# Kernel tuning notes

Hardware: AMD Instinct MI355X
Metric: run time of the kernel (lower is better)

The kernel has to match this reference:

```python
import jax, jax.numpy as jnp
import numpy as np

B, N, C = 4, 2048, 768
H = 12
D = C // H  # head_dim = 64
SCALE = D ** -0.5


def setup_inputs() -> dict:
    key = jax.random.key(0)
    ks = jax.random.split(key, 9)
    x = jax.random.normal(ks[0], (B, N, C), dtype=jnp.float32)
    k_in = jax.random.normal(ks[1], (B, N, C), dtype=jnp.float32)
    v_in = jax.random.normal(ks[2], (B, N, C), dtype=jnp.float32)
    rel_pos_bias = jax.random.normal(ks[3], (H, N, N), dtype=jnp.float32)
    # learned params (nn.Linear stores weight [out, in]; y = x @ W.T + b)
    s = C ** -0.5
    Wq = jax.random.normal(ks[4], (C, C), dtype=jnp.float32) * s
    Wk = jax.random.normal(ks[5], (C, C), dtype=jnp.float32) * s
    Wv = jax.random.normal(ks[6], (C, C), dtype=jnp.float32) * s
    Wp = jax.random.normal(ks[7], (C, C), dtype=jnp.float32) * s
    bp = jax.random.normal(ks[8], (C,), dtype=jnp.float32) * 0.01
    return {"x": x, "k_in": k_in, "v_in": v_in, "rel_pos_bias": rel_pos_bias,
            "Wq": Wq, "Wk": Wk, "Wv": Wv, "Wp": Wp, "bp": bp}


def reference(x, k_in, v_in, rel_pos_bias, Wq, Wk, Wv, Wp, bp):
    # linear projections (no q/k/v bias since qkv_bias=False)
    q = jnp.einsum('bnc,dc->bnd', x, Wq)      # [B,N,C]
    k = jnp.einsum('bnc,dc->bnd', k_in, Wk)   # [B,Nk,C]
    v = jnp.einsum('bnc,dc->bnd', v_in, Wv)   # [B,Nv,C]
    # split heads -> [B,H,N,D]
    q = q.reshape(B, N, H, D).transpose(0, 2, 1, 3) * SCALE
    k = k.reshape(B, -1, H, D).transpose(0, 2, 1, 3)
    v = v.reshape(B, -1, H, D).transpose(0, 2, 1, 3)
    attn = jnp.einsum('bhnd,bhmd->bhnm', q, k)          # [B,H,N,Nk]
    attn = attn + rel_pos_bias[None]                    # additive rel-pos bias
    attn = jax.nn.softmax(attn, axis=-1)
    out = jnp.einsum('bhnm,bhmd->bhnd', attn, v)        # [B,H,N,D]
    out = out.transpose(0, 2, 1, 3).reshape(B, N, C)
    return jnp.einsum('bnc,dc->bnd', out, Wp) + bp
```

## Files before the change

### kernel.cpp

```cpp
#include <hip/hip_runtime.h>
#include <stdint.h>
#include <stddef.h>

#define B_ 4
#define N_ 2048
#define C_ 768
#define H_ 12
#define M_ (B_ * N_)

typedef __attribute__((ext_vector_type(8))) short bf16x8_t;
typedef __attribute__((ext_vector_type(4))) float f32x4_t;

__device__ __forceinline__ unsigned pack2_bf16(float f0, float f1) {
  unsigned u0 = __builtin_bit_cast(unsigned, f0) + 0x8000u;
  unsigned u1 = __builtin_bit_cast(unsigned, f1) + 0x8000u;
  return __builtin_amdgcn_perm(u1, u0, 0x07060302u);
}

__device__ __forceinline__ short f2bf(float f) {
  unsigned u = __builtin_bit_cast(unsigned, f);
  u = (u + 0x7FFFu + ((u >> 16) & 1u)) >> 16;
  return (short)u;
}
__device__ __forceinline__ short f2bf_fast(float f) {
  return (short)((__builtin_bit_cast(unsigned, f) + 0x8000u) >> 16);
}

__device__ __forceinline__ void gload_lds16(const short* g, const short* l) {
  __builtin_amdgcn_global_load_lds(
      (const __attribute__((address_space(1))) void*)g,
      (__attribute__((address_space(3))) void*)l, 16, 0, 0);
}

#define XV 1572864
#define WV 147456
__global__ __launch_bounds__(256) void cvt_all(
    const float* __restrict__ x, const float* __restrict__ kin, const float* __restrict__ vin,
    const float* __restrict__ wq, const float* __restrict__ wk, const float* __restrict__ wv,
    const float* __restrict__ wp,
    unsigned short* __restrict__ xb, unsigned short* __restrict__ kb, unsigned short* __restrict__ vb,
    unsigned short* __restrict__ wqb, unsigned short* __restrict__ wkb, unsigned short* __restrict__ wvb,
    unsigned short* __restrict__ wpb)
{
  int i = blockIdx.x * 256 + threadIdx.x;
  const float* s; unsigned short* d; int off;
  if      (i < XV)            { s = x;   d = xb;  off = i; }
  else if (i < 2 * XV)        { s = kin; d = kb;  off = i - XV; }
  else if (i < 3 * XV)        { s = vin; d = vb;  off = i - 2 * XV; }
  else if (i < 3 * XV + WV)   { s = wq;  d = wqb; off = i - 3 * XV; }
  else if (i < 3 * XV + 2*WV) { s = wk;  d = wkb; off = i - 3 * XV - WV; }
  else if (i < 3 * XV + 3*WV) { s = wv;  d = wvb; off = i - 3 * XV - 2 * WV; }
  else                        { s = wp;  d = wpb; off = i - 3 * XV - 3 * WV; }
  float4 v = ((const float4*)s)[off];
  uint2 p;
  p.x = pack2_bf16(v.x, v.y);
  p.y = pack2_bf16(v.z, v.w);
  ((uint2*)d)[off] = p;
}

__global__ __launch_bounds__(256) void proj_qkv(
    const short* __restrict__ xb, const short* __restrict__ kb, const short* __restrict__ vb,
    const short* __restrict__ wqb, const short* __restrict__ wkb, const short* __restrict__ wvb,
    short* __restrict__ q_ws, short* __restrict__ k_ws, short* __restrict__ vt_ws)
{
  const int z = blockIdx.z;
  const short* A = (z == 0) ? xb : (z == 1) ? kb : vb;
  const short* W = (z == 0) ? wqb : (z == 1) ? wkb : wvb;
  const int m0 = blockIdx.x * 128;
  const int n0 = blockIdx.y * 128;

  __shared__ __align__(16) short smem[128 * 136];
  short* As = smem;
  short* Bs = smem + 128 * 64;

  const int t = threadIdx.x;
  const int w = t >> 6, L = t & 63, L15 = L & 15, quad = L >> 4;
  const int wm = w & 1, wn = w >> 1;

  f32x4_t acc[4][4] = {};

  const short* ga = A + (size_t)(m0 + w * 32 + (L >> 3)) * C_ + (L & 7) * 8;
  const short* gb = W + (size_t)(n0 + w * 32 + (L >> 3)) * C_ + (L & 7) * 8;
  const short* la = As + (w * 32) * 64;
  const short* lb = Bs + (w * 32) * 64;

  for (int k0 = 0; k0 < C_; k0 += 64) {
    __syncthreads();
    #pragma unroll
    for (int i = 0; i < 4; ++i) {
      gload_lds16(ga + (size_t)i * 8 * C_ + k0, la + i * 512);
      gload_lds16(gb + (size_t)i * 8 * C_ + k0, lb + i * 512);
    }
    __syncthreads();
    #pragma unroll
    for (int kk = 0; kk < 2; ++kk) {
      bf16x8_t af[4], bf[4];
      #pragma unroll
      for (int mt = 0; mt < 4; ++mt)
        af[mt] = *(const bf16x8_t*)&As[(wm * 64 + mt * 16 + L15) * 64 + kk * 32 + quad * 8];
      #pragma unroll
      for (int nt = 0; nt < 4; ++nt)
        bf[nt] = *(const bf16x8_t*)&Bs[(wn * 64 + nt * 16 + L15) * 64 + kk * 32 + quad * 8];
      #pragma unroll
      for (int mt = 0; mt < 4; ++mt)
        #pragma unroll
        for (int nt = 0; nt < 4; ++nt)
          acc[mt][nt] = __builtin_amdgcn_mfma_f32_16x16x32_bf16(af[mt], bf[nt], acc[mt][nt], 0, 0, 0);
    }
  }

  if (z != 2) {
    short* outp = (z == 0) ? q_ws : k_ws;
    const float mul = (z == 0) ? 0.125f : 1.0f;
    #pragma unroll
    for (int mt = 0; mt < 4; ++mt) {
      const int m_base = m0 + wm * 64 + mt * 16 + quad * 4;
      #pragma unroll
      for (int nt = 0; nt < 4; ++nt) {
        const int c = n0 + wn * 64 + nt * 16 + L15;
        const int h = c >> 6, d = c & 63;
        #pragma unroll
        for (int r = 0; r < 4; ++r) {
          const int m = m_base + r;
          const int b = m >> 11, n = m & 2047;
          outp[((size_t)(b * H_ + h) * N_ + n) * 64 + d] = f2bf(acc[mt][nt][r] * mul);
        }
      }
    }
  } else {
    __syncthreads();
    #pragma unroll
    for (int mt = 0; mt < 4; ++mt) {
      const int ml = wm * 64 + mt * 16 + quad * 4;
      #pragma unroll
      for (int nt = 0; nt < 4; ++nt) {
        const int cl = wn * 64 + nt * 16 + L15;
        #pragma unroll
        for (int r = 0; r < 4; ++r)
          smem[cl * 136 + ml + r] = f2bf(acc[mt][nt][r]);
      }
    }
    __syncthreads();
    const int bb = m0 >> 11;
    const int nn0 = m0 & 2047;
    #pragma unroll
    for (int pp = 0; pp < 8; ++pp) {
      const int cl = pp * 16 + (t >> 4);
      const int mg = t & 15;
      const uint4 val = *(const uint4*)&smem[cl * 136 + mg * 8];
      const int cg = n0 + cl;
      *(uint4*)&vt_ws[(((size_t)(bb * H_ + (cg >> 6))) * 64 + (cg & 63)) * N_ + nn0 + mg * 8] = val;
    }
  }
}

__global__ __launch_bounds__(256, 3) void attn(
    const short* __restrict__ q_ws, const short* __restrict__ k_ws,
    const short* __restrict__ vt_ws, const float* __restrict__ rpb,
    short* __restrict__ attn_out)
{
  const int p  = blockIdx.x;
  const int lw = (p & 7) * 96 + (p >> 3);
  const int h  = lw >> 6;
  const int xl = lw & 63;
  const int b  = xl & 3;
  const int m0 = (xl >> 2) * 128;
  const int bh = b * H_ + h;

  __shared__ __align__(16) short Ks [64 * 64];
  __shared__ __align__(16) short Vts[64 * 64];
  __shared__ __align__(16) short Ps [4][32 * 64];

  const int t = threadIdx.x;
  const int w = t >> 6, L = t & 63, L15 = L & 15, quad = L >> 4;
  const int sr  = t >> 2;
  const int scb = (t & 3) << 5;
  const int swz_w = (sr & 7) << 4;

  const short* qp  = q_ws  + ((size_t)bh * N_ + m0) * 64;
  const short* kp  = k_ws  + (size_t)bh * N_ * 64;
  const short* vtp = vt_ws + (size_t)bh * 64 * N_;
  const float* bpb = rpb + (size_t)h * N_ * N_;

  bf16x8_t aq[2][2];
  #pragma unroll
  for (int mt = 0; mt < 2; ++mt)
    #pragma unroll
    for (int kk = 0; kk < 2; ++kk)
      aq[mt][kk] = *(const bf16x8_t*)(qp + (size_t)(w * 32 + mt * 16 + L15) * 64 + kk * 32 + quad * 8);

  f32x4_t o[2][4] = {};
  float psum[2][4] = {};

  for (int kv0 = 0; kv0 < N_; kv0 += 64) {
    __syncthreads();
    {
      const short* gk = kp + (size_t)(kv0 + sr) * 64 + (scb >> 1);
      const uint4 k0 = *(const uint4*)gk;
      const uint4 k1 = *(const uint4*)(gk + 8);
      const short* gv = vtp + (size_t)sr * N_ + kv0 + (scb >> 1);
      const uint4 v0 = *(const uint4*)gv;
      const uint4 v1 = *(const uint4*)(gv + 8);
      *(uint4*)((char*)Ks  + sr * 128 + (scb ^ swz_w))        = k0;
      *(uint4*)((char*)Ks  + sr * 128 + ((scb + 16) ^ swz_w)) = k1;
      *(uint4*)((char*)Vts + sr * 128 + (scb ^ swz_w))        = v0;
      *(uint4*)((char*)Vts + sr * 128 + ((scb + 16) ^ swz_w)) = v1;
    }
    float bias[2][4][4];
    {
      const float* bq = bpb + (size_t)(m0 + w * 32 + quad * 4) * N_ + kv0 + L15;
      #pragma unroll
      for (int mt = 0; mt < 2; ++mt)
        #pragma unroll
        for (int r = 0; r < 4; ++r)
          #pragma unroll
          for (int nt = 0; nt < 4; ++nt)
            bias[mt][nt][r] = bq[(size_t)(mt * 16 + r) * N_ + nt * 16];
    }
    __syncthreads();

    f32x4_t s[2][4];
    #pragma unroll
    for (int nt = 0; nt < 4; ++nt) {
      const int row = nt * 16 + L15;
      const char* kbp = (const char*)Ks + row * 128;
      const int sx = (row & 7) << 4;
      const bf16x8_t b0 = *(const bf16x8_t*)(kbp + ((quad * 16) ^ sx));
      const bf16x8_t b1 = *(const bf16x8_t*)(kbp + ((64 + quad * 16) ^ sx));
      #pragma unroll
      for (int mt = 0; mt < 2; ++mt) {
        f32x4_t sv = {bias[mt][nt][0], bias[mt][nt][1], bias[mt][nt][2], bias[mt][nt][3]};
        sv = __builtin_amdgcn_mfma_f32_16x16x32_bf16(aq[mt][0], b0, sv, 0, 0, 0);
        s[mt][nt] = __builtin_amdgcn_mfma_f32_16x16x32_bf16(aq[mt][1], b1, sv, 0, 0, 0);
      }
    }

    #pragma unroll
    for (int mt = 0; mt < 2; ++mt)
      #pragma unroll
      for (int nt = 0; nt < 4; ++nt)
        #pragma unroll
        for (int r = 0; r < 4; ++r) {
          const float e = __expf(s[mt][nt][r]);
          psum[mt][r] += e;
          const int qrow = mt * 16 + quad * 4 + r;
          const int cb = (nt * 32 + L15 * 2) ^ ((qrow & 7) << 4);
          *(short*)((char*)Ps[w] + qrow * 128 + cb) = f2bf_fast(e);
        }

    #pragma unroll
    for (int kk = 0; kk < 2; ++kk) {
      bf16x8_t pa[2];
      #pragma unroll
      for (int mt = 0; mt < 2; ++mt) {
        const int row = mt * 16 + L15;
        pa[mt] = *(const bf16x8_t*)((char*)Ps[w] + row * 128 +
                                    ((kk * 64 + quad * 16) ^ ((row & 7) << 4)));
      }
      #pragma unroll
      for (int nt = 0; nt < 4; ++nt) {
        const int row = nt * 16 + L15;
        const bf16x8_t vbf = *(const bf16x8_t*)((char*)Vts + row * 128 +
                                                ((kk * 64 + quad * 16) ^ ((row & 7) << 4)));
        #pragma unroll
        for (int mt = 0; mt < 2; ++mt)
          o[mt][nt] = __builtin_amdgcn_mfma_f32_16x16x32_bf16(pa[mt], vbf, o[mt][nt], 0, 0, 0);
      }
    }
  }

  #pragma unroll
  for (int mt = 0; mt < 2; ++mt)
    #pragma unroll
    for (int r = 0; r < 4; ++r) {
      float v = psum[mt][r];
      v += __shfl_xor(v, 1);
      v += __shfl_xor(v, 2);
      v += __shfl_xor(v, 4);
      v += __shfl_xor(v, 8);
      psum[mt][r] = 1.0f / v;
    }

  #pragma unroll
  for (int mt = 0; mt < 2; ++mt) {
    const int n_base = m0 + w * 32 + mt * 16 + quad * 4;
    #pragma unroll
    for (int nt = 0; nt < 4; ++nt)
      #pragma unroll
      for (int r = 0; r < 4; ++r) {
        const float v = o[mt][nt][r] * psum[mt][r];
        attn_out[((size_t)(b * N_ + n_base + r)) * C_ + h * 64 + nt * 16 + L15] = f2bf(v);
      }
  }
}

__global__ __launch_bounds__(256) void proj_out(
    const short* __restrict__ Abf, const short* __restrict__ wpb,
    const float* __restrict__ bpv, float* __restrict__ out)
{
  const int m0 = blockIdx.x * 128;
  const int n0 = blockIdx.y * 128;

  __shared__ short As[128 * 64];
  __shared__ short Bs[128 * 64];

  const int t = threadIdx.x;
  const int w = t >> 6, L = t & 63, L15 = L & 15, quad = L >> 4;
  const int wm = w & 1, wn = w >> 1;

  f32x4_t acc[4][4] = {};

  const short* ga = Abf + (size_t)(m0 + w * 32 + (L >> 3)) * C_ + (L & 7) * 8;
  const short* gb = wpb + (size_t)(n0 + w * 32 + (L >> 3)) * C_ + (L & 7) * 8;
  const short* la = &As[(w * 32) * 64];
  const short* lb = &Bs[(w * 32) * 64];

  for (int k0 = 0; k0 < C_; k0 += 64) {
    __syncthreads();
    #pragma unroll
    for (int i = 0; i < 4; ++i) {
      gload_lds16(ga + (size_t)i * 8 * C_ + k0, la + i * 512);
      gload_lds16(gb + (size_t)i * 8 * C_ + k0, lb + i * 512);
    }
    __syncthreads();
    #pragma unroll
    for (int kk = 0; kk < 2; ++kk) {
      bf16x8_t af[4], bf[4];
      #pragma unroll
      for (int mt = 0; mt < 4; ++mt)
        af[mt] = *(const bf16x8_t*)&As[(wm * 64 + mt * 16 + L15) * 64 + kk * 32 + quad * 8];
      #pragma unroll
      for (int nt = 0; nt < 4; ++nt)
        bf[nt] = *(const bf16x8_t*)&Bs[(wn * 64 + nt * 16 + L15) * 64 + kk * 32 + quad * 8];
      #pragma unroll
      for (int mt = 0; mt < 4; ++mt)
        #pragma unroll
        for (int nt = 0; nt < 4; ++nt)
          acc[mt][nt] = __builtin_amdgcn_mfma_f32_16x16x32_bf16(af[mt], bf[nt], acc[mt][nt], 0, 0, 0);
    }
  }

  #pragma unroll
  for (int mt = 0; mt < 4; ++mt) {
    const int m_base = m0 + wm * 64 + mt * 16 + quad * 4;
    #pragma unroll
    for (int nt = 0; nt < 4; ++nt) {
      const int c = n0 + wn * 64 + nt * 16 + L15;
      const float bb = bpv[c];
      #pragma unroll
      for (int r = 0; r < 4; ++r)
        out[(size_t)(m_base + r) * C_ + c] = acc[mt][nt][r] + bb;
    }
  }
}

extern "C" void kernel_launch(void* const* d_in, const int* in_sizes, int n_in,
                              void* d_out, int out_size, void* d_ws, size_t ws_size,
                              hipStream_t stream) {
  const float* x    = (const float*)d_in[0];
  const float* k_in = (const float*)d_in[1];
  const float* v_in = (const float*)d_in[2];
  const float* rpb  = (const float*)d_in[3];
  const float* Wq   = (const float*)d_in[4];
  const float* Wk   = (const float*)d_in[5];
  const float* Wv   = (const float*)d_in[6];
  const float* Wp   = (const float*)d_in[7];
  const float* bp   = (const float*)d_in[8];
  float* out = (float*)d_out;

  const size_t SZ = (size_t)B_ * H_ * N_ * 64 * sizeof(short);
  const size_t WSZ = (size_t)C_ * C_ * sizeof(short);
  char* ws = (char*)d_ws;
  short* q_ws  = (short*)(ws);
  short* k_ws  = (short*)(ws + SZ);
  short* vt_ws = (short*)(ws + 2 * SZ);
  short* ao_ws = (short*)(ws + 3 * SZ);
  short* xb    = (short*)(ws + 4 * SZ);
  short* kb    = (short*)(ws + 5 * SZ);
  short* vb    = (short*)(ws + 6 * SZ);
  short* wqb   = (short*)(ws + 7 * SZ);
  short* wkb   = (short*)(ws + 7 * SZ + WSZ);
  short* wvb   = (short*)(ws + 7 * SZ + 2 * WSZ);
  short* wpb   = (short*)(ws + 7 * SZ + 3 * WSZ);

  cvt_all<<<(3 * XV + 4 * WV + 255) / 256, 256, 0, stream>>>(
      x, k_in, v_in, Wq, Wk, Wv, Wp,
      (unsigned short*)xb, (unsigned short*)kb, (unsigned short*)vb,
      (unsigned short*)wqb, (unsigned short*)wkb, (unsigned short*)wvb, (unsigned short*)wpb);
  proj_qkv<<<dim3(M_ / 128, C_ / 128, 3), 256, 0, stream>>>(
      xb, kb, vb, wqb, wkb, wvb, q_ws, k_ws, vt_ws);
  attn<<<dim3(B_ * (N_ / 128) * H_), 256, 0, stream>>>(q_ws, k_ws, vt_ws, rpb, ao_ws);
  proj_out<<<dim3(M_ / 128, C_ / 128), 256, 0, stream>>>(ao_ws, wpb, bp, out);
}
```

Measured before the change: 473.0 us.

## Double-buffer K/V tiles with direct global-to-LDS loads and prefetch bias

The attention kernel now keeps two LDS buffers for the K and V^T tiles and fills them with direct global-to-LDS loads (gload_lds16). The next tile is issued while the current one is being computed, and the loop needs only one barrier per iteration. Bias values for the next tile are loaded into registers after the QK MFMAs, which hides the latency of the large relative-position-bias stream. MFMA sections are wrapped in s_setprio raises. The cost is doubled LDS for K/V and more live registers, and the change depends on gload_lds16 handling its wait counts correctly before the barrier.

```diff
diff --git a/kernel.cpp b/kernel.cpp
--- a/kernel.cpp
+++ b/kernel.cpp
@@ -167,21 +167,23 @@
   const int m0 = (xl >> 2) * 128;
   const int bh = b * H_ + h;
 
-  __shared__ __align__(16) short Ks [64 * 64];
-  __shared__ __align__(16) short Vts[64 * 64];
+  __shared__ __align__(16) short Ks [2][64 * 64];
+  __shared__ __align__(16) short Vts[2][64 * 64];
   __shared__ __align__(16) short Ps [4][32 * 64];
 
   const int t = threadIdx.x;
   const int w = t >> 6, L = t & 63, L15 = L & 15, quad = L >> 4;
-  const int sr  = t >> 2;
-  const int scb = (t & 3) << 5;
-  const int swz_w = (sr & 7) << 4;
 
   const short* qp  = q_ws  + ((size_t)bh * N_ + m0) * 64;
   const short* kp  = k_ws  + (size_t)bh * N_ * 64;
   const short* vtp = vt_ws + (size_t)bh * 64 * N_;
   const float* bpb = rpb + (size_t)h * N_ * N_;
 
+  const int srow8 = L >> 3;
+  const int scolS = ((L & 7) ^ srow8) * 8;
+  const short* gk_base = kp  + (size_t)(w * 16 + srow8) * 64 + scolS;
+  const short* gv_base = vtp + (size_t)(w * 16 + srow8) * N_ + scolS;
+
   bf16x8_t aq[2][2];
   #pragma unroll
   for (int mt = 0; mt < 2; ++mt)
@@ -189,41 +191,44 @@
     for (int kk = 0; kk < 2; ++kk)
       aq[mt][kk] = *(const bf16x8_t*)(qp + (size_t)(w * 32 + mt * 16 + L15) * 64 + kk * 32 + quad * 8);
 
+  const float* bq = bpb + (size_t)(m0 + w * 32 + quad * 4) * N_ + L15;
+
   f32x4_t o[2][4] = {};
   float psum[2][4] = {};
-
-  for (int kv0 = 0; kv0 < N_; kv0 += 64) {
-    __syncthreads();
-    {
-      const short* gk = kp + (size_t)(kv0 + sr) * 64 + (scb >> 1);
-      const uint4 k0 = *(const uint4*)gk;
-      const uint4 k1 = *(const uint4*)(gk + 8);
-      const short* gv = vtp + (size_t)sr * N_ + kv0 + (scb >> 1);
-      const uint4 v0 = *(const uint4*)gv;
-      const uint4 v1 = *(const uint4*)(gv + 8);
-      *(uint4*)((char*)Ks  + sr * 128 + (scb ^ swz_w))        = k0;
-      *(uint4*)((char*)Ks  + sr * 128 + ((scb + 16) ^ swz_w)) = k1;
-      *(uint4*)((char*)Vts + sr * 128 + (scb ^ swz_w))        = v0;
-      *(uint4*)((char*)Vts + sr * 128 + ((scb + 16) ^ swz_w)) = v1;
-    }
-    float bias[2][4][4];
-    {
-      const float* bq = bpb + (size_t)(m0 + w * 32 + quad * 4) * N_ + kv0 + L15;
-      #pragma unroll
-      for (int mt = 0; mt < 2; ++mt)
-        #pragma unroll
-        for (int r = 0; r < 4; ++r)
-          #pragma unroll
-          for (int nt = 0; nt < 4; ++nt)
-            bias[mt][nt][r] = bq[(size_t)(mt * 16 + r) * N_ + nt * 16];
-    }
-    __syncthreads();
+  float bias[2][4][4];
+
+  #pragma unroll
+  for (int i = 0; i < 2; ++i) {
+    gload_lds16(gk_base + (size_t)i * 8 * 64, &Ks[0][w * 1024 + i * 512]);
+    gload_lds16(gv_base + (size_t)i * 8 * N_, &Vts[0][w * 1024 + i * 512]);
+  }
+  #pragma unroll
+  for (int mt = 0; mt < 2; ++mt)
+    #pragma unroll
+    for (int r = 0; r < 4; ++r)
+      #pragma unroll
+      for (int nt = 0; nt < 4; ++nt)
+        bias[mt][nt][r] = bq[(size_t)(mt * 16 + r) * N_ + nt * 16];
+  __syncthreads();
+
+  for (int T = 0; T < 32; ++T) {
+    const int cur = T & 1, nxt = cur ^ 1;
+
+    if (T < 31) {
+      const int kv1 = (T + 1) * 64;
+      #pragma unroll
+      for (int i = 0; i < 2; ++i) {
+        gload_lds16(gk_base + (size_t)(kv1 + i * 8) * 64, &Ks[nxt][w * 1024 + i * 512]);
+        gload_lds16(gv_base + (size_t)i * 8 * N_ + kv1,   &Vts[nxt][w * 1024 + i * 512]);
+      }
+    }
 
     f32x4_t s[2][4];
+    __builtin_amdgcn_s_setprio(1);
     #pragma unroll
     for (int nt = 0; nt < 4; ++nt) {
       const int row = nt * 16 + L15;
-      const char* kbp = (const char*)Ks + row * 128;
+      const char* kbp = (const char*)Ks[cur] + row * 128;
       const int sx = (row & 7) << 4;
       const bf16x8_t b0 = *(const bf16x8_t*)(kbp + ((quad * 16) ^ sx));
       const bf16x8_t b1 = *(const bf16x8_t*)(kbp + ((64 + quad * 16) ^ sx));
@@ -233,6 +238,18 @@
         sv = __builtin_amdgcn_mfma_f32_16x16x32_bf16(aq[mt][0], b0, sv, 0, 0, 0);
         s[mt][nt] = __builtin_amdgcn_mfma_f32_16x16x32_bf16(aq[mt][1], b1, sv, 0, 0, 0);
       }
+    }
+    __builtin_amdgcn_s_setprio(0);
+
+    if (T < 31) {
+      const float* bqn = bq + (size_t)(T + 1) * 64;
+      #pragma unroll
+      for (int mt = 0; mt < 2; ++mt)
+        #pragma unroll
+        for (int r = 0; r < 4; ++r)
+          #pragma unroll
+          for (int nt = 0; nt < 4; ++nt)
+            bias[mt][nt][r] = bqn[(size_t)(mt * 16 + r) * N_ + nt * 16];
     }
 
     #pragma unroll
@@ -248,6 +265,7 @@
           *(short*)((char*)Ps[w] + qrow * 128 + cb) = f2bf_fast(e);
         }
 
+    __builtin_amdgcn_s_setprio(1);
     #pragma unroll
     for (int kk = 0; kk < 2; ++kk) {
       bf16x8_t pa[2];
@@ -260,13 +278,16 @@
       #pragma unroll
       for (int nt = 0; nt < 4; ++nt) {
         const int row = nt * 16 + L15;
-        const bf16x8_t vbf = *(const bf16x8_t*)((char*)Vts + row * 128 +
+        const bf16x8_t vbf = *(const bf16x8_t*)((char*)Vts[cur] + row * 128 +
                                                 ((kk * 64 + quad * 16) ^ ((row & 7) << 4)));
         #pragma unroll
         for (int mt = 0; mt < 2; ++mt)
           o[mt][nt] = __builtin_amdgcn_mfma_f32_16x16x32_bf16(pa[mt], vbf, o[mt][nt], 0, 0, 0);
       }
     }
+    __builtin_amdgcn_s_setprio(0);
+
+    __syncthreads();
   }
 
   #pragma unroll
```

New measurement: 465.7 us. About the same (-1.6%).
